# Kernel optimization log

Hardware: AMD Instinct MI355X
Metric: run time of the kernel (lower is better)

The kernel has to match this reference:

```python
import jax, jax.numpy as jnp
import numpy as np

HEAD = 16
DIM = 1024
HEAD_DIM = DIM // HEAD


def setup_inputs() -> dict:
    key = jax.random.key(0)
    k1, k2, k3, k4 = jax.random.split(key, 4)
    x = jax.random.normal(k1, (2, 2048, DIM), dtype=jnp.float32)
    # nn.Linear(dim, 3*dim, bias=False): weight [3*dim, dim]
    w_qkv = jax.random.normal(k2, (3 * DIM, DIM), dtype=jnp.float32) * (DIM ** -0.5)
    # output proj nn.Linear(dim, dim)
    w_out = jax.random.normal(k3, (DIM, DIM), dtype=jnp.float32) * (DIM ** -0.5)
    b_out = jax.random.normal(k4, (DIM,), dtype=jnp.float32) * 0.01
    return {"x": x, "w_qkv": w_qkv, "w_out": w_out, "b_out": b_out}


def reference(x, w_qkv, w_out, b_out):
    b, s, _ = x.shape
    scale = HEAD_DIM ** -0.5
    qkv = jnp.einsum('bsd,ed->bse', x, w_qkv)  # [b, s, 3*dim]
    q, k, v = jnp.split(qkv, 3, axis=-1)
    def split_heads(t):
        return t.reshape(b, s, HEAD, HEAD_DIM).transpose(0, 2, 1, 3)  # b h s d
    q, k, v = split_heads(q), split_heads(k), split_heads(v)
    scores = jnp.einsum('bhqd,bhkd->bhqk', q, k) * scale
    attn = jax.nn.softmax(scores, axis=-1)
    out = jnp.einsum('bhqk,bhkd->bhqd', attn, v)
    out = out.transpose(0, 2, 1, 3).reshape(b, s, DIM)
    out = jnp.einsum('bsd,ed->bse', out, w_out) + b_out
    return out
```

## Files before the change

### kernel.cpp

```cpp
#include <hip/hip_runtime.h>
#include <hip/hip_bf16.h>
#include <stdint.h>

typedef __bf16 bf16_t;
typedef __attribute__((ext_vector_type(8))) __bf16 bf16x8;
typedef __attribute__((ext_vector_type(4))) __bf16 bf16x4v;
typedef __attribute__((ext_vector_type(4))) float f32x4;

#define GLOBAL_AS __attribute__((address_space(1)))
#define LDS_AS __attribute__((address_space(3)))

__device__ __forceinline__ void gload_lds16(const bf16_t* g, bf16_t* l) {
  __builtin_amdgcn_global_load_lds((const GLOBAL_AS void*)g, (LDS_AS void*)l, 16, 0, 0);
}

__device__ __forceinline__ uint32_t pk2(float a, float b) {
  union { bf16_t h[2]; uint32_t u; } x;
  x.h[0] = (bf16_t)a; x.h[1] = (bf16_t)b;
  return x.u;
}

__device__ __forceinline__ bf16x8 xpose8(bf16x8 v, int l) {
  union { bf16x8 v; uint32_t u[4]; } tv; tv.v = v;
  uint32_t a0 = __shfl_xor((int)tv.u[2], 4, 64);
  uint32_t a1 = __shfl_xor((int)tv.u[3], 4, 64);
  uint32_t a2 = __shfl_xor((int)tv.u[0], 4, 64);
  uint32_t a3 = __shfl_xor((int)tv.u[1], 4, 64);
  bool s4 = (l & 4) != 0;
  uint32_t n0 = s4 ? a0 : tv.u[0];
  uint32_t n1 = s4 ? a1 : tv.u[1];
  uint32_t n2 = s4 ? tv.u[2] : a2;
  uint32_t n3 = s4 ? tv.u[3] : a3;
  uint32_t b0 = __shfl_xor((int)n1, 2, 64);
  uint32_t b1 = __shfl_xor((int)n0, 2, 64);
  uint32_t b2 = __shfl_xor((int)n3, 2, 64);
  uint32_t b3 = __shfl_xor((int)n2, 2, 64);
  bool s2 = (l & 2) != 0;
  uint32_t m0 = s2 ? b0 : n0;
  uint32_t m1 = s2 ? n1 : b1;
  uint32_t m2 = s2 ? b2 : n2;
  uint32_t m3 = s2 ? n3 : b3;
  uint32_t c0 = __shfl_xor((int)m0, 1, 64);
  uint32_t c1 = __shfl_xor((int)m1, 1, 64);
  uint32_t c2 = __shfl_xor((int)m2, 1, 64);
  uint32_t c3 = __shfl_xor((int)m3, 1, 64);
  bool odd = (l & 1) != 0;
  union { uint32_t u[4]; bf16x8 v; } tw;
  tw.u[0] = odd ? ((m0 & 0xFFFF0000u) | (c0 >> 16)) : ((m0 & 0xFFFFu) | (c0 << 16));
  tw.u[1] = odd ? ((m1 & 0xFFFF0000u) | (c1 >> 16)) : ((m1 & 0xFFFFu) | (c1 << 16));
  tw.u[2] = odd ? ((m2 & 0xFFFF0000u) | (c2 >> 16)) : ((m2 & 0xFFFFu) | (c2 << 16));
  tw.u[3] = odd ? ((m3 & 0xFFFF0000u) | (c3 >> 16)) : ((m3 & 0xFFFFu) | (c3 << 16));
  return tw.v;
}

__global__ void cvt_f32_bf16(const float* __restrict__ in, bf16_t* __restrict__ out, int n) {
  int i = (blockIdx.x * 256 + threadIdx.x) * 4;
  if (i + 3 < n) {
    float4 v = *(const float4*)(in + i);
    bf16x4v o;
    o[0] = (bf16_t)v.x; o[1] = (bf16_t)v.y; o[2] = (bf16_t)v.z; o[3] = (bf16_t)v.w;
    *(bf16x4v*)(out + i) = o;
  }
}

template<int EPI>
__global__ __launch_bounds__(256)
void gemm_tn(const bf16_t* __restrict__ A, const bf16_t* __restrict__ B,
             void* __restrict__ Cout, const float* __restrict__ bias,
             int K, int ldc, int qcols, float qscale)
{
  __shared__ __align__(16) bf16_t As[128 * 32];
  __shared__ __align__(16) bf16_t Bs[128 * 32];
  const int t  = threadIdx.x;
  const int l  = t & 63, w = t >> 6;
  const int wm = w >> 1, wn = w & 1;
  const int lo = l & 15, hi = l >> 4;
  const int brow = blockIdx.y * 128;
  const int bcol = blockIdx.x * 128;

  const int i0 = t, i1 = t + 256;
  const int r0 = i0 >> 2, c0 = i0 & 3;
  const int r1 = i1 >> 2, c1 = i1 & 3;

  f32x4 acc[4][4] = {};

  for (int k0 = 0; k0 < K; k0 += 32) {
    gload_lds16(A + (size_t)(brow + r0) * K + k0 + c0 * 8, As + i0 * 8);
    gload_lds16(A + (size_t)(brow + r1) * K + k0 + c1 * 8, As + i1 * 8);
    gload_lds16(B + (size_t)(bcol + r0) * K + k0 + c0 * 8, Bs + i0 * 8);
    gload_lds16(B + (size_t)(bcol + r1) * K + k0 + c1 * 8, Bs + i1 * 8);
    __syncthreads();

    bf16x8 a[4], bb[4];
#pragma unroll
    for (int fm = 0; fm < 4; fm++)
      a[fm] = *(const bf16x8*)(As + (wm * 64 + fm * 16 + lo) * 32 + hi * 8);
#pragma unroll
    for (int fn = 0; fn < 4; fn++)
      bb[fn] = *(const bf16x8*)(Bs + (wn * 64 + fn * 16 + lo) * 32 + hi * 8);

#pragma unroll
    for (int fm = 0; fm < 4; fm++)
#pragma unroll
      for (int fn = 0; fn < 4; fn++)
        acc[fm][fn] = __builtin_amdgcn_mfma_f32_16x16x32_bf16(a[fm], bb[fn], acc[fm][fn], 0, 0, 0);
    __syncthreads();
  }

#pragma unroll
  for (int fm = 0; fm < 4; fm++) {
#pragma unroll
    for (int fn = 0; fn < 4; fn++) {
#pragma unroll
      for (int j = 0; j < 4; j++) {
        int row = brow + wm * 64 + fm * 16 + hi * 4 + j;
        int col = bcol + wn * 64 + fn * 16 + lo;
        float v = acc[fm][fn][j];
        if (EPI == 0) {
          if (col < qcols) v *= qscale;
          ((bf16_t*)Cout)[(size_t)row * ldc + col] = (bf16_t)v;
        } else {
          ((float*)Cout)[(size_t)row * ldc + col] = v + bias[col];
        }
      }
    }
  }
}

#define LDK 72

__global__ __launch_bounds__(256, 2)
void flash_attn(const bf16_t* __restrict__ qkv, bf16_t* __restrict__ aout)
{
  __shared__ __align__(16) bf16_t Kl[2][64 * LDK];
  __shared__ __align__(16) bf16_t Vt[2][64 * LDK];

  const int t = threadIdx.x;
  const int l = t & 63, w = t >> 6;
  const int lo = l & 15, hi = l >> 4;
  int bid = (int)blockIdx.x;
  bid = (bid & 7) * 64 + (bid >> 3);
  const int qblk = bid & 15;
  const int bh   = bid >> 4;
  const int b = bh >> 4, h = bh & 15;
  const int rowbase = b * 2048;
  const int q0 = qblk * 128 + w * 32;

  const int r = l & 7, c = l >> 3;
  const int krow_w = w * 16 + r;
  const int vkey_w = 32 * (w >> 1) + 8 * (w & 1) + 16 * (r >> 2) + (r & 3);
  const bf16_t* kvbase = qkv + (size_t)rowbase * 3072 + h * 64 + 1024;
  const size_t step = (size_t)64 * 3072;

  bf16x8 aq[2][2];
#pragma unroll
  for (int fm = 0; fm < 2; fm++)
#pragma unroll
    for (int kb = 0; kb < 2; kb++)
      aq[fm][kb] = *(const bf16x8*)(qkv + (size_t)(rowbase + q0 + fm * 16 + lo) * 3072
                                    + h * 64 + kb * 32 + hi * 8);

  bf16x8 ones;
#pragma unroll
  for (int j = 0; j < 8; j++) ones[j] = (bf16_t)1.0f;

  f32x4 oacc[2][4] = {};
  f32x4 ssum[2] = {};

  bf16x8 kch[2], vch[2];
#pragma unroll
  for (int i = 0; i < 2; i++) {
    kch[i] = *(const bf16x8*)(kvbase + (size_t)(krow_w + 8 * i) * 3072 + c * 8);
    vch[i] = *(const bf16x8*)(kvbase + 1024 + (size_t)(vkey_w + 4 * i) * 3072 + c * 8);
  }
#pragma unroll
  for (int i = 0; i < 2; i++) {
    *(bf16x8*)(&Kl[0][0] + (krow_w + 8 * i) * LDK + c * 8) = kch[i];
    *(bf16x8*)(&Vt[0][0] + (c * 8 + r) * LDK + w * 16 + i * 8) = xpose8(vch[i], l);
  }
  const bf16_t* kv_next = kvbase + step;
#pragma unroll
  for (int i = 0; i < 2; i++) {
    kch[i] = *(const bf16x8*)(kv_next + (size_t)(krow_w + 8 * i) * 3072 + c * 8);
    vch[i] = *(const bf16x8*)(kv_next + 1024 + (size_t)(vkey_w + 4 * i) * 3072 + c * 8);
  }
  kv_next += step;

  for (int it = 0; it < 32; ++it) {
    __syncthreads();
    const int cur = it & 1;
    bf16_t* KlN = &Kl[cur ^ 1][0];
    bf16_t* VtN = &Vt[cur ^ 1][0];
    const bf16_t* KlC = &Kl[cur][0];
    const bf16_t* VtC = &Vt[cur][0];

    if (it < 31) {
#pragma unroll
      for (int i = 0; i < 2; i++) {
        *(bf16x8*)(KlN + (krow_w + 8 * i) * LDK + c * 8) = kch[i];
        *(bf16x8*)(VtN + (c * 8 + r) * LDK + w * 16 + i * 8) = xpose8(vch[i], l);
      }
    }
    if (it < 30) {
#pragma unroll
      for (int i = 0; i < 2; i++) {
        kch[i] = *(const bf16x8*)(kv_next + (size_t)(krow_w + 8 * i) * 3072 + c * 8);
        vch[i] = *(const bf16x8*)(kv_next + 1024 + (size_t)(vkey_w + 4 * i) * 3072 + c * 8);
      }
      kv_next += step;
    }

    bf16x8 kf[4][2];
#pragma unroll
    for (int fn = 0; fn < 4; fn++)
#pragma unroll
      for (int kb = 0; kb < 2; kb++)
        kf[fn][kb] = *(const bf16x8*)(KlC + (fn * 16 + lo) * LDK + kb * 32 + hi * 8);
    f32x4 sacc[2][4] = {};
#pragma unroll
    for (int fm = 0; fm < 2; fm++)
#pragma unroll
      for (int fn = 0; fn < 4; fn++)
#pragma unroll
        for (int kb = 0; kb < 2; kb++)
          sacc[fm][fn] = __builtin_amdgcn_mfma_f32_16x16x32_bf16(kf[fn][kb], aq[fm][kb], sacc[fm][fn], 0, 0, 0);

    bf16x8 pa[2][2];
#pragma unroll
    for (int fm = 0; fm < 2; fm++) {
      float p[4][4];
#pragma unroll
      for (int fn = 0; fn < 4; fn++)
#pragma unroll
        for (int j = 0; j < 4; j++)
          p[fn][j] = __builtin_amdgcn_exp2f(sacc[fm][fn][j]);
#pragma unroll
      for (int kb = 0; kb < 2; kb++) {
        union { uint32_t u[4]; bf16x8 v; } pw;
        pw.u[0] = pk2(p[2 * kb][0],     p[2 * kb][1]);
        pw.u[1] = pk2(p[2 * kb][2],     p[2 * kb][3]);
        pw.u[2] = pk2(p[2 * kb + 1][0], p[2 * kb + 1][1]);
        pw.u[3] = pk2(p[2 * kb + 1][2], p[2 * kb + 1][3]);
        pa[fm][kb] = pw.v;
      }
    }

    bf16x8 vb[4][2];
#pragma unroll
    for (int fd = 0; fd < 4; fd++)
#pragma unroll
      for (int kb = 0; kb < 2; kb++)
        vb[fd][kb] = *(const bf16x8*)(VtC + (fd * 16 + lo) * LDK + kb * 32 + hi * 8);
#pragma unroll
    for (int fm = 0; fm < 2; fm++)
#pragma unroll
      for (int kb = 0; kb < 2; kb++)
        ssum[fm] = __builtin_amdgcn_mfma_f32_16x16x32_bf16(pa[fm][kb], ones, ssum[fm], 0, 0, 0);
#pragma unroll
    for (int fm = 0; fm < 2; fm++)
#pragma unroll
      for (int fd = 0; fd < 4; fd++)
#pragma unroll
        for (int kb = 0; kb < 2; kb++)
          oacc[fm][fd] = __builtin_amdgcn_mfma_f32_16x16x32_bf16(pa[fm][kb], vb[fd][kb], oacc[fm][fd], 0, 0, 0);
  }

#pragma unroll
  for (int fm = 0; fm < 2; fm++)
#pragma unroll
    for (int j = 0; j < 4; j++) {
      float inv = 1.0f / ssum[fm][j];
      int row = rowbase + q0 + fm * 16 + hi * 4 + j;
#pragma unroll
      for (int fd = 0; fd < 4; fd++) {
        int col = h * 64 + fd * 16 + lo;
        aout[(size_t)row * 1024 + col] = (bf16_t)(oacc[fm][fd][j] * inv);
      }
    }
}

extern "C" void kernel_launch(void* const* d_in, const int* in_sizes, int n_in,
                              void* d_out, int out_size, void* d_ws, size_t ws_size,
                              hipStream_t stream) {
  const float* x     = (const float*)d_in[0];
  const float* w_qkv = (const float*)d_in[1];
  const float* w_out = (const float*)d_in[2];
  const float* b_out = (const float*)d_in[3];

  char* ws = (char*)d_ws;
  bf16_t* xb   = (bf16_t*)(ws);
  bf16_t* wqb  = (bf16_t*)(ws + 8388608);
  bf16_t* wob  = (bf16_t*)(ws + 14680064);
  bf16_t* qkvb = (bf16_t*)(ws + 16777216);
  bf16_t* aob  = (bf16_t*)(ws + 41943040);

  cvt_f32_bf16<<<4096, 256, 0, stream>>>(x,     xb,  4194304);
  cvt_f32_bf16<<<3072, 256, 0, stream>>>(w_qkv, wqb, 3145728);
  cvt_f32_bf16<<<1024, 256, 0, stream>>>(w_out, wob, 1048576);

  dim3 g1(24, 32);
  gemm_tn<0><<<g1, 256, 0, stream>>>(xb, wqb, qkvb, nullptr, 1024, 3072, 1024, 0.18033688011f);

  flash_attn<<<512, 256, 0, stream>>>(qkvb, aob);

  dim3 g2(8, 32);
  gemm_tn<1><<<g2, 256, 0, stream>>>(aob, wob, d_out, b_out, 1024, 1024, 0, 1.0f);
}
```

Baseline: 144.7 us.

## Use 8 waves per attention block with 16 query rows each, add MFMA priority

The flash attention block grows from 4 to 8 waves, each wave now owning 16 query rows instead of 32, and the K/V tile staging is redistributed so each thread loads one chunk instead of two. This halves per-wave register state and raises the number of waves available to hide latency. It also wraps the MFMA sections in s_setprio. In exchange, each K/V fragment read from LDS now feeds only half as many MFMAs, so LDS traffic per unit of compute roughly doubles.

```diff
diff --git a/kernel.cpp b/kernel.cpp
--- a/kernel.cpp
+++ b/kernel.cpp
@@ -129,7 +129,7 @@
 
 #define LDK 72
 
-__global__ __launch_bounds__(256, 2)
+__global__ __launch_bounds__(512, 4)
 void flash_attn(const bf16_t* __restrict__ qkv, bf16_t* __restrict__ aout)
 {
   __shared__ __align__(16) bf16_t Kl[2][64 * LDK];
@@ -144,46 +144,36 @@
   const int bh   = bid >> 4;
   const int b = bh >> 4, h = bh & 15;
   const int rowbase = b * 2048;
-  const int q0 = qblk * 128 + w * 32;
+  const int q0 = qblk * 128 + w * 16;
 
   const int r = l & 7, c = l >> 3;
-  const int krow_w = w * 16 + r;
-  const int vkey_w = 32 * (w >> 1) + 8 * (w & 1) + 16 * (r >> 2) + (r & 3);
+  const int krow = w * 8 + (l >> 3);
+  const int kc   = l & 7;
+  const int vkey = 32 * (w >> 2) + 16 * (r >> 2) + 4 * (w & 3) + (r & 3);
   const bf16_t* kvbase = qkv + (size_t)rowbase * 3072 + h * 64 + 1024;
   const size_t step = (size_t)64 * 3072;
 
-  bf16x8 aq[2][2];
-#pragma unroll
-  for (int fm = 0; fm < 2; fm++)
-#pragma unroll
-    for (int kb = 0; kb < 2; kb++)
-      aq[fm][kb] = *(const bf16x8*)(qkv + (size_t)(rowbase + q0 + fm * 16 + lo) * 3072
-                                    + h * 64 + kb * 32 + hi * 8);
+  bf16x8 aq[2];
+#pragma unroll
+  for (int kb = 0; kb < 2; kb++)
+    aq[kb] = *(const bf16x8*)(qkv + (size_t)(rowbase + q0 + lo) * 3072
+                              + h * 64 + kb * 32 + hi * 8);
 
   bf16x8 ones;
 #pragma unroll
   for (int j = 0; j < 8; j++) ones[j] = (bf16_t)1.0f;
 
-  f32x4 oacc[2][4] = {};
-  f32x4 ssum[2] = {};
-
-  bf16x8 kch[2], vch[2];
-#pragma unroll
-  for (int i = 0; i < 2; i++) {
-    kch[i] = *(const bf16x8*)(kvbase + (size_t)(krow_w + 8 * i) * 3072 + c * 8);
-    vch[i] = *(const bf16x8*)(kvbase + 1024 + (size_t)(vkey_w + 4 * i) * 3072 + c * 8);
-  }
-#pragma unroll
-  for (int i = 0; i < 2; i++) {
-    *(bf16x8*)(&Kl[0][0] + (krow_w + 8 * i) * LDK + c * 8) = kch[i];
-    *(bf16x8*)(&Vt[0][0] + (c * 8 + r) * LDK + w * 16 + i * 8) = xpose8(vch[i], l);
-  }
+  f32x4 oacc[4] = {};
+  f32x4 ssum = {};
+
+  bf16x8 kch = *(const bf16x8*)(kvbase + (size_t)krow * 3072 + kc * 8);
+  bf16x8 vch = *(const bf16x8*)(kvbase + 1024 + (size_t)vkey * 3072 + c * 8);
+  *(bf16x8*)(&Kl[0][0] + krow * LDK + kc * 8) = kch;
+  *(bf16x8*)(&Vt[0][0] + (c * 8 + r) * LDK + w * 8) = xpose8(vch, l);
+
   const bf16_t* kv_next = kvbase + step;
-#pragma unroll
-  for (int i = 0; i < 2; i++) {
-    kch[i] = *(const bf16x8*)(kv_next + (size_t)(krow_w + 8 * i) * 3072 + c * 8);
-    vch[i] = *(const bf16x8*)(kv_next + 1024 + (size_t)(vkey_w + 4 * i) * 3072 + c * 8);
-  }
+  kch = *(const bf16x8*)(kv_next + (size_t)krow * 3072 + kc * 8);
+  vch = *(const bf16x8*)(kv_next + 1024 + (size_t)vkey * 3072 + c * 8);
   kv_next += step;
 
   for (int it = 0; it < 32; ++it) {
@@ -195,18 +185,12 @@
     const bf16_t* VtC = &Vt[cur][0];
 
     if (it < 31) {
-#pragma unroll
-      for (int i = 0; i < 2; i++) {
-        *(bf16x8*)(KlN + (krow_w + 8 * i) * LDK + c * 8) = kch[i];
-        *(bf16x8*)(VtN + (c * 8 + r) * LDK + w * 16 + i * 8) = xpose8(vch[i], l);
-      }
+      *(bf16x8*)(KlN + krow * LDK + kc * 8) = kch;
+      *(bf16x8*)(VtN + (c * 8 + r) * LDK + w * 8) = xpose8(vch, l);
     }
     if (it < 30) {
-#pragma unroll
-      for (int i = 0; i < 2; i++) {
-        kch[i] = *(const bf16x8*)(kv_next + (size_t)(krow_w + 8 * i) * 3072 + c * 8);
-        vch[i] = *(const bf16x8*)(kv_next + 1024 + (size_t)(vkey_w + 4 * i) * 3072 + c * 8);
-      }
+      kch = *(const bf16x8*)(kv_next + (size_t)krow * 3072 + kc * 8);
+      vch = *(const bf16x8*)(kv_next + 1024 + (size_t)vkey * 3072 + c * 8);
       kv_next += step;
     }
 
@@ -216,33 +200,30 @@
 #pragma unroll
       for (int kb = 0; kb < 2; kb++)
         kf[fn][kb] = *(const bf16x8*)(KlC + (fn * 16 + lo) * LDK + kb * 32 + hi * 8);
-    f32x4 sacc[2][4] = {};
-#pragma unroll
-    for (int fm = 0; fm < 2; fm++)
-#pragma unroll
-      for (int fn = 0; fn < 4; fn++)
-#pragma unroll
-        for (int kb = 0; kb < 2; kb++)
-          sacc[fm][fn] = __builtin_amdgcn_mfma_f32_16x16x32_bf16(kf[fn][kb], aq[fm][kb], sacc[fm][fn], 0, 0, 0);
-
-    bf16x8 pa[2][2];
-#pragma unroll
-    for (int fm = 0; fm < 2; fm++) {
-      float p[4][4];
-#pragma unroll
-      for (int fn = 0; fn < 4; fn++)
-#pragma unroll
-        for (int j = 0; j < 4; j++)
-          p[fn][j] = __builtin_amdgcn_exp2f(sacc[fm][fn][j]);
-#pragma unroll
-      for (int kb = 0; kb < 2; kb++) {
-        union { uint32_t u[4]; bf16x8 v; } pw;
-        pw.u[0] = pk2(p[2 * kb][0],     p[2 * kb][1]);
-        pw.u[1] = pk2(p[2 * kb][2],     p[2 * kb][3]);
-        pw.u[2] = pk2(p[2 * kb + 1][0], p[2 * kb + 1][1]);
-        pw.u[3] = pk2(p[2 * kb + 1][2], p[2 * kb + 1][3]);
-        pa[fm][kb] = pw.v;
-      }
+    f32x4 sacc[4] = {};
+    __builtin_amdgcn_s_setprio(1);
+#pragma unroll
+    for (int fn = 0; fn < 4; fn++)
+#pragma unroll
+      for (int kb = 0; kb < 2; kb++)
+        sacc[fn] = __builtin_amdgcn_mfma_f32_16x16x32_bf16(kf[fn][kb], aq[kb], sacc[fn], 0, 0, 0);
+    __builtin_amdgcn_s_setprio(0);
+
+    float p[4][4];
+#pragma unroll
+    for (int fn = 0; fn < 4; fn++)
+#pragma unroll
+      for (int j = 0; j < 4; j++)
+        p[fn][j] = __builtin_amdgcn_exp2f(sacc[fn][j]);
+    bf16x8 pa[2];
+#pragma unroll
+    for (int kb = 0; kb < 2; kb++) {
+      union { uint32_t u[4]; bf16x8 v; } pw;
+      pw.u[0] = pk2(p[2 * kb][0],     p[2 * kb][1]);
+      pw.u[1] = pk2(p[2 * kb][2],     p[2 * kb][3]);
+      pw.u[2] = pk2(p[2 * kb + 1][0], p[2 * kb + 1][1]);
+      pw.u[3] = pk2(p[2 * kb + 1][2], p[2 * kb + 1][3]);
+      pa[kb] = pw.v;
     }
 
     bf16x8 vb[4][2];
@@ -251,32 +232,28 @@
 #pragma unroll
       for (int kb = 0; kb < 2; kb++)
         vb[fd][kb] = *(const bf16x8*)(VtC + (fd * 16 + lo) * LDK + kb * 32 + hi * 8);
-#pragma unroll
-    for (int fm = 0; fm < 2; fm++)
-#pragma unroll
-      for (int kb = 0; kb < 2; kb++)
-        ssum[fm] = __builtin_amdgcn_mfma_f32_16x16x32_bf16(pa[fm][kb], ones, ssum[fm], 0, 0, 0);
-#pragma unroll
-    for (int fm = 0; fm < 2; fm++)
-#pragma unroll
-      for (int fd = 0; fd < 4; fd++)
-#pragma unroll
-        for (int kb = 0; kb < 2; kb++)
-          oacc[fm][fd] = __builtin_amdgcn_mfma_f32_16x16x32_bf16(pa[fm][kb], vb[fd][kb], oacc[fm][fd], 0, 0, 0);
-  }
-
-#pragma unroll
-  for (int fm = 0; fm < 2; fm++)
-#pragma unroll
-    for (int j = 0; j < 4; j++) {
-      float inv = 1.0f / ssum[fm][j];
-      int row = rowbase + q0 + fm * 16 + hi * 4 + j;
-#pragma unroll
-      for (int fd = 0; fd < 4; fd++) {
-        int col = h * 64 + fd * 16 + lo;
-        aout[(size_t)row * 1024 + col] = (bf16_t)(oacc[fm][fd][j] * inv);
-      }
-    }
+    __builtin_amdgcn_s_setprio(1);
+#pragma unroll
+    for (int kb = 0; kb < 2; kb++)
+      ssum = __builtin_amdgcn_mfma_f32_16x16x32_bf16(pa[kb], ones, ssum, 0, 0, 0);
+#pragma unroll
+    for (int fd = 0; fd < 4; fd++)
+#pragma unroll
+      for (int kb = 0; kb < 2; kb++)
+        oacc[fd] = __builtin_amdgcn_mfma_f32_16x16x32_bf16(pa[kb], vb[fd][kb], oacc[fd], 0, 0, 0);
+    __builtin_amdgcn_s_setprio(0);
+  }
+
+#pragma unroll
+  for (int j = 0; j < 4; j++) {
+    float inv = 1.0f / ssum[j];
+    int row = rowbase + q0 + hi * 4 + j;
+#pragma unroll
+    for (int fd = 0; fd < 4; fd++) {
+      int col = h * 64 + fd * 16 + lo;
+      aout[(size_t)row * 1024 + col] = (bf16_t)(oacc[fd][j] * inv);
+    }
+  }
 }
 
 extern "C" void kernel_launch(void* const* d_in, const int* in_sizes, int n_in,
@@ -301,7 +278,7 @@
   dim3 g1(24, 32);
   gemm_tn<0><<<g1, 256, 0, stream>>>(xb, wqb, qkvb, nullptr, 1024, 3072, 1024, 0.18033688011f);
 
-  flash_attn<<<512, 256, 0, stream>>>(qkvb, aob);
+  flash_attn<<<512, 512, 0, stream>>>(qkvb, aob);
 
   dim3 g2(8, 32);
   gemm_tn<1><<<g2, 256, 0, stream>>>(aob, wob, d_out, b_out, 1024, 1024, 0, 1.0f);
```

New measurement: 141.1 us. 1.03x faster.
